# Kernel tuning notes

Hardware: AMD Instinct MI355X
Metric: run time of the kernel (lower is better)

Reference implementation:

```python
import jax, jax.numpy as jnp
import numpy as np

D_MODEL = 512
NUM_HEADS = 4
KEY_DIM = 512          # expand_k = 1.0
VALUE_DIM = 1024       # expand_v = 2.0
HEAD_QK = KEY_DIM // NUM_HEADS    # 128
HEAD_V = VALUE_DIM // NUM_HEADS   # 256
GATE_LOW_RANK = 16
GATE_LOGIT_NORMALIZER = 16
EPS = 1e-5
CHUNK = 64
B, HH, WW = 8, 56, 56
N = HH * WW


def rmsnorm(x, w, eps=EPS):
    return x * jax.lax.rsqrt(jnp.mean(x * x, axis=-1, keepdims=True) + eps) * w


def gla_chunk(q, k, v, gk, scale, chunk=CHUNK):
    """Chunked gated linear attention (causal, decay gate on key dim).
    q,k,gk: [B,H,N,dk], v: [B,H,N,dv]. Recurrence:
      S_t = diag(exp(gk_t)) S_{t-1} + k_t^T v_t ;  o_t = (q_t*scale) S_t
    """
    Bb, Hh, Nn, dk = q.shape
    dv = v.shape[-1]
    nc = Nn // chunk

    def rc(t):  # [B,H,N,d] -> [nc,B,H,chunk,d]
        return jnp.moveaxis(t.reshape(Bb, Hh, nc, chunk, t.shape[-1]), 2, 0)

    qs, ks, vs, gs = rc(q), rc(k), rc(v), rc(gk)
    b = jnp.cumsum(gs, axis=-2)  # inclusive intra-chunk log-decay
    mask = jnp.tril(jnp.ones((chunk, chunk), bool))

    def step(S, inp):
        q_, k_, v_, b_ = inp
        qe = q_ * jnp.exp(b_) * scale                      # [B,H,C,dk]
        A = jnp.einsum('bhtd,bhsd->bhts', qe, k_ * jnp.exp(-b_))
        A = jnp.where(mask, A, 0.0)                        # causal intra-chunk
        o = jnp.einsum('bhts,bhsv->bhtv', A, v_) \
            + jnp.einsum('bhtd,bhdv->bhtv', qe, S)         # inter-chunk
        btot = b_[..., -1:, :]                             # [B,H,1,dk]
        S = S * jnp.exp(btot[..., 0, :])[..., None] \
            + jnp.einsum('bhtd,bhtv->bhdv', k_ * jnp.exp(btot - b_), v_)
        return S, o

    S0 = jnp.zeros((Bb, Hh, dk, dv), q.dtype)
    _, os = jax.lax.scan(step, S0, (qs, ks, vs, b))
    return jnp.moveaxis(os, 0, 2).reshape(Bb, Hh, Nn, dv)


def setup_inputs() -> dict:
    key = jax.random.key(0)
    ks = jax.random.split(key, 9)
    s = 0.02
    return {
        'x': jax.random.normal(ks[0], (B, N, D_MODEL), jnp.float32),
        'conv_w': jax.random.normal(ks[1], (D_MODEL, 1, 3, 3), jnp.float32) * s,
        'qkv_w': jax.random.normal(ks[2], (2 * KEY_DIM + VALUE_DIM, D_MODEL), jnp.float32) * s,
        'gk_w1': jax.random.normal(ks[3], (GATE_LOW_RANK, D_MODEL), jnp.float32) * s,
        'gk_w2': jax.random.normal(ks[4], (2 * KEY_DIM, GATE_LOW_RANK), jnp.float32) * s,
        'gk_b2': jax.random.normal(ks[5], (2 * KEY_DIM,), jnp.float32) * s,
        'g_w': jax.random.normal(ks[6], (VALUE_DIM, D_MODEL), jnp.float32) * s,
        'g_b': jax.random.normal(ks[7], (VALUE_DIM,), jnp.float32) * s,
        'gnorm_w': jnp.ones((HEAD_V,), jnp.float32),
        'lnorm_w': jnp.ones((HEAD_V,), jnp.float32),
        'o_w': jax.random.normal(ks[8], (D_MODEL, VALUE_DIM), jnp.float32) * s,
        'hw_h': HH,
        'hw_w': WW,
    }


def reference(x, conv_w, qkv_w, gk_w1, gk_w2, gk_b2, g_w, g_b,
              gnorm_w, lnorm_w, o_w, hw_h, hw_w):
    Bb, Nn, C = x.shape
    # in_proj: depthwise 3x3 conv over spatial layout + SiLU
    x2d = x.reshape(Bb, hw_h, hw_w, C).transpose(0, 3, 1, 2)
    x2d = jax.lax.conv_general_dilated(
        x2d, conv_w, (1, 1), 'SAME',
        dimension_numbers=('NCHW', 'OIHW', 'NCHW'), feature_group_count=C)
    xs = jax.nn.silu(x2d).transpose(0, 2, 3, 1).reshape(Bb, Nn, C)

    qkv = xs @ qkv_w.T
    q, k, v = jnp.split(qkv, [KEY_DIM, 2 * KEY_DIM], axis=-1)

    def heads(t, d):  # [B,N,h*d] -> [B,h,N,d]
        return t.reshape(Bb, Nn, NUM_HEADS, d).transpose(0, 2, 1, 3)

    q, k, v = heads(q, HEAD_QK), heads(k, HEAD_QK), heads(v, HEAD_V)

    # low-rank gate projection, two groups (forward / backward scan)
    gk = (xs @ gk_w1.T) @ gk_w2.T + gk_b2
    gk = jax.nn.log_sigmoid(gk) / GATE_LOGIT_NORMALIZER
    gk_f, gk_b = jnp.split(gk, 2, axis=-1)
    gk_f, gk_b = heads(gk_f, HEAD_QK), heads(gk_b, HEAD_QK)

    scale = HEAD_QK ** -0.5
    o_f = gla_chunk(q, k, v, gk_f, scale)
    flip = lambda t: t[:, :, ::-1]
    o_b = flip(gla_chunk(flip(q), flip(k), flip(v), flip(gk_b), scale))

    o = rmsnorm(o_f, gnorm_w) + rmsnorm(o_b, lnorm_w)   # [B,h,N,dv]
    o = o.transpose(0, 2, 1, 3).reshape(Bb, Nn, VALUE_DIM)
    g = xs @ g_w.T + g_b
    o = jax.nn.silu(g) * o                              # swish output gate
    return o @ o_w.T
```

## Files before the change

kernel.cpp:

```cpp
#include <hip/hip_runtime.h>
#include <hip/hip_bf16.h>
#include <math.h>

#define NHEADS 4
#define DMODEL 512
#define HQK 128
#define HV 256
#define BBATCH 8
#define SH 56
#define SWW 56
#define SEQN (SH*SWW)
#define NTOK (BBATCH*SEQN)
#define CH2 32
#define NC2 (SEQN/CH2)


typedef __bf16 bf16x8 __attribute__((ext_vector_type(8)));
typedef float  f32x4  __attribute__((ext_vector_type(4)));

__device__ __forceinline__ float silu_f(float v){ return v / (1.f + __expf(-v)); }

__device__ __forceinline__ float b2f(unsigned short u){
  union { unsigned int i; float f; } c; c.i = ((unsigned int)u) << 16; return c.f;
}
__device__ __forceinline__ unsigned short f2b(float f){
  __bf16 h = (__bf16)f;
  unsigned short u; __builtin_memcpy(&u, &h, 2); return u;
}
__device__ __forceinline__ float h2f(unsigned short u){
  _Float16 h; __builtin_memcpy(&h, &u, 2); return (float)h;
}
__device__ __forceinline__ unsigned short f2h(float f){
  _Float16 h = (_Float16)f; unsigned short u; __builtin_memcpy(&u, &h, 2); return u;
}
__device__ __forceinline__ float lsig16(float z){
  float e = __expf(-fabsf(z));
  return (fminf(z, 0.f) - __logf(1.f + e)) * 0.0625f;
}
__device__ __forceinline__ void up8(uint4 v, unsigned short* o){
  o[0]=(unsigned short)v.x; o[1]=(unsigned short)(v.x>>16);
  o[2]=(unsigned short)v.y; o[3]=(unsigned short)(v.y>>16);
  o[4]=(unsigned short)v.z; o[5]=(unsigned short)(v.z>>16);
  o[6]=(unsigned short)v.w; o[7]=(unsigned short)(v.w>>16);
}
__device__ __forceinline__ uint4 pk8(const unsigned short* s){
  uint4 v;
  v.x = (unsigned)s[0] | ((unsigned)s[1]<<16);
  v.y = (unsigned)s[2] | ((unsigned)s[3]<<16);
  v.z = (unsigned)s[4] | ((unsigned)s[5]<<16);
  v.w = (unsigned)s[6] | ((unsigned)s[7]<<16);
  return v;
}

#define GLL16(gp, lp) __builtin_amdgcn_global_load_lds( \
    (const __attribute__((address_space(1))) unsigned int*)(gp), \
    (__attribute__((address_space(3))) unsigned int*)(lp), 16, 0, 0)

__global__ __launch_bounds__(256) void k_w2b(const float* __restrict__ w,
                                             unsigned short* __restrict__ o, int n){
  int i = (blockIdx.x*256 + threadIdx.x) << 2;
  if (i >= n) return;
  float4 v = *(const float4*)&w[i];
  ushort4 p;
  p.x = f2b(v.x); p.y = f2b(v.y); p.z = f2b(v.z); p.w = f2b(v.w);
  *(ushort4*)&o[i] = p;
}

__global__ __launch_bounds__(256) void k_wc(const float* __restrict__ w1,
                                            const float* __restrict__ w2,
                                            unsigned short* __restrict__ wc){
  int idx = blockIdx.x*256 + threadIdx.x;
  int n = idx >> 9, k = idx & 511;
  float acc = 0.f;
  #pragma unroll
  for (int r=0;r<16;++r) acc += w2[n*16+r]*w1[r*512+k];
  wc[idx] = f2b(acc);
}

__global__ __launch_bounds__(256) void k_conv_silu(const float* __restrict__ x,
                                                   const float* __restrict__ cw,
                                                   unsigned short* __restrict__ xs){
  int gid = blockIdx.x*256 + threadIdx.x;
  int c4  = (gid & 127) << 2;
  int tok = gid >> 7;
  int b = tok / SEQN, sp = tok % SEQN;
  int hh = sp / SWW, ww = sp % SWW;
  float a0=0.f,a1=0.f,a2=0.f,a3=0.f;
  #pragma unroll
  for (int dh=-1; dh<=1; ++dh){
    int h2 = hh+dh; if (h2<0||h2>=SH) continue;
    #pragma unroll
    for (int dw=-1; dw<=1; ++dw){
      int w2 = ww+dw; if (w2<0||w2>=SWW) continue;
      const float4 xv = *(const float4*)&x[((size_t)(b*SEQN + h2*SWW + w2))*DMODEL + c4];
      int tap = (dh+1)*3 + (dw+1);
      a0 += xv.x * cw[(c4+0)*9 + tap];
      a1 += xv.y * cw[(c4+1)*9 + tap];
      a2 += xv.z * cw[(c4+2)*9 + tap];
      a3 += xv.w * cw[(c4+3)*9 + tap];
    }
  }
  ushort4 o;
  o.x = f2b(silu_f(a0)); o.y = f2b(silu_f(a1)); o.z = f2b(silu_f(a2)); o.w = f2b(silu_f(a3));
  *(ushort4*)&xs[(size_t)tok*DMODEL + c4] = o;
}

template<int ACT, int CBF>
__global__ __launch_bounds__(256) void k_gemm_mfma(const unsigned short* __restrict__ A,
                                                   const unsigned short* __restrict__ W,
                                                   const float* __restrict__ bias,
                                                   void* __restrict__ Cv,
                                                   int M, int N, int K){
  __shared__ unsigned short sA[128*32];
  __shared__ unsigned short sB[128*32];
  const int tid  = threadIdx.x;
  const int wave = tid >> 6, lane = tid & 63;
  const int lm = lane & 15, quad = lane >> 4;
  const int wm = wave & 1, wn = wave >> 1;
  const int m0 = blockIdx.y * 128, n0 = blockIdx.x * 128;

  const int r0 = tid >> 2,  c0 = (tid & 3) << 3;
  const int f1 = tid + 256;
  const int r1 = f1 >> 2,   c1 = (f1 & 3) << 3;

  f32x4 acc[4][4] = {};

  for (int kt = 0; kt < K; kt += 32){
    GLL16(&A[(size_t)(m0 + r0)*K + kt + c0], &sA[(size_t)tid*8]);
    GLL16(&A[(size_t)(m0 + r1)*K + kt + c1], &sA[(size_t)f1*8]);
    GLL16(&W[(size_t)(n0 + r0)*K + kt + c0], &sB[(size_t)tid*8]);
    GLL16(&W[(size_t)(n0 + r1)*K + kt + c1], &sB[(size_t)f1*8]);
    __syncthreads();
    bf16x8 af[4], bf[4];
    #pragma unroll
    for (int i=0;i<4;++i) af[i] = *(const bf16x8*)&sA[(wm*64 + i*16 + lm)*32 + quad*8];
    #pragma unroll
    for (int j=0;j<4;++j) bf[j] = *(const bf16x8*)&sB[(wn*64 + j*16 + lm)*32 + quad*8];
    #pragma unroll
    for (int i=0;i<4;++i)
      #pragma unroll
      for (int j=0;j<4;++j)
        acc[i][j] = __builtin_amdgcn_mfma_f32_16x16x32_bf16(af[i], bf[j], acc[i][j], 0, 0, 0);
    __syncthreads();
  }

  #pragma unroll
  for (int i=0;i<4;++i){
    #pragma unroll
    for (int r=0;r<4;++r){
      size_t m = (size_t)(m0 + wm*64 + i*16 + quad*4 + r);
      #pragma unroll
      for (int j=0;j<4;++j){
        int n = n0 + wn*64 + j*16 + lm;
        float v = acc[i][j][r];
        if (bias) v += bias[n];
        if (ACT==1) v = silu_f(v);
        if (CBF) ((unsigned short*)Cv)[m*(size_t)N + n] = f2b(v);
        else     ((float*)Cv)[m*(size_t)N + n] = v;
      }
    }
  }
}

__global__ __launch_bounds__(256) void k_prep(unsigned short* __restrict__ qkv,
                                              const unsigned short* __restrict__ z,
                                              unsigned short* __restrict__ dbuf,
                                              unsigned short* __restrict__ ebF,
                                              unsigned short* __restrict__ ebB){
  const int blk = blockIdx.x;
  const int bb = blk / NC2, cB = blk % NC2;
  const int j  = threadIdx.x << 1;
  const int cb = j & 0x180;
  const int sl = j & 127;
  const int d1 = ((sl & 7) << 4) | (sl >> 3);
  const int d2 = d1 + 16;
  const size_t base = (size_t)bb*SEQN + cB*CH2;
  const float sc = 0.08838834764831845f;
  float bf0[CH2], bf1[CH2];
  float r0 = 0.f, r1 = 0.f;
  #pragma unroll
  for (int t=0;t<CH2;++t){
    size_t tok = base + t;
    float z0 = b2f(z[tok*1024 + cb + d1]);
    float z1 = b2f(z[tok*1024 + cb + d2]);
    r0 += lsig16(z0);
    r1 += lsig16(z1);
    bf0[t] = r0; bf1[t] = r1;
    float qv1 = b2f(qkv[tok*2048 + cb + d1]);
    float qv2 = b2f(qkv[tok*2048 + cb + d2]);
    float kv1 = b2f(qkv[tok*2048 + 512 + cb + d1]);
    float kv2 = b2f(qkv[tok*2048 + 512 + cb + d2]);
    float e0 = __expf(r0),  e1 = __expf(r1);
    float n0 = __expf(-r0), n1 = __expf(-r1);
    unsigned qo = (unsigned)f2b(qv1*e0*sc) | ((unsigned)f2b(qv2*e1*sc) << 16);
    unsigned ko = (unsigned)f2b(kv1*n0)    | ((unsigned)f2b(kv2*n1) << 16);
    __syncthreads();
    *(unsigned*)&qkv[tok*2048 + j] = qo;
    *(unsigned*)&qkv[tok*2048 + 512 + j] = ko;
  }
  const int hh = j >> 7;
  {
    int ef = ((bb*NHEADS + hh)*NC2 + cB)*HQK;
    ebF[ef + d1] = f2h(__expf(bf0[CH2-1]));
    ebF[ef + d2] = f2h(__expf(bf1[CH2-1]));
  }
  r0 = 0.f; r1 = 0.f;
  #pragma unroll
  for (int t=CH2-1;t>=0;--t){
    size_t tok = base + t;
    float z0 = b2f(z[tok*1024 + 512 + cb + d1]);
    float z1 = b2f(z[tok*1024 + 512 + cb + d2]);
    r0 += lsig16(z0);
    r1 += lsig16(z1);
    float dd0 = r0 - bf0[t], dd1 = r1 - bf1[t];
    *(unsigned*)&dbuf[tok*512 + j] = (unsigned)f2h(__expf(dd0))
                                   | ((unsigned)f2h(__expf(dd1)) << 16);
  }
  {
    int eb = ((bb*NHEADS + hh)*NC2 + (NC2-1-cB))*HQK;
    ebB[eb + d1] = f2h(__expf(r0));
    ebB[eb + d2] = f2h(__expf(r1));
  }
}

#define SKET_STORE(sKeT_, kb_, o8_, ts_) \
  _Pragma("unroll") \
  for (int u=0;u<8;++u){ \
    (sKeT_)[(u*16 + 2*(o8_)    )*40 + (ts_)] = (kb_)[u]; \
    (sKeT_)[(u*16 + 2*(o8_) + 1)*40 + (ts_)] = (kb_)[u+8]; \
  }

__global__ __launch_bounds__(256) void k_gla_state(const unsigned short* __restrict__ qkvb,
                                                   const unsigned short* __restrict__ dbuf,
                                                   const unsigned short* __restrict__ ebFt,
                                                   const unsigned short* __restrict__ ebBt,
                                                   float* __restrict__ dSseg){
  __shared__ __align__(16) unsigned short sKeT[128*40];
  __shared__ __align__(16) unsigned short sVT[64*40];
  __shared__ float sEb[128];

  const int tid = threadIdx.x;
  const int bx = blockIdx.x;
  const int combo = bx & 255, seg = bx >> 8;
  const int vq = combo & 3, dir = (combo>>2)&1, hh = (combo>>3)&3, bb = (combo>>5)&7;

  const int w = tid >> 6, lane = tid & 63;
  const int quad = lane >> 4, lm = lane & 15;
  const int ts = tid >> 3, o8 = tid & 7, d16 = o8 << 4;
  const int tl = tid & 31, vg = tid >> 5;

  const int kcol = 512 + hh*HQK, vcol = 1024 + hh*HV + vq*64;
  const int dcol = hh*HQK;
  const unsigned short* ebT = dir ? ebBt : ebFt;
  const int ebBase = (bb*NHEADS + hh)*NC2*HQK;
  const int c0 = (seg==0)?0:(seg==1)?13:(seg==2)?25:(seg==3)?37:(seg==4)?50:62;
  const int c1 = (seg==0)?13:(seg==1)?25:(seg==2)?37:(seg==3)?50:(seg==4)?62:74;

  f32x4 Sreg[8];
  #pragma unroll
  for (int i=0;i<8;++i){
    #pragma unroll
    for (int r=0;r<4;++r) Sreg[i][r] = 0.f;
  }

  for (int c = c0; c < c1; ++c){
    {
      int p = c*CH2 + ts;
      int n = dir ? (SEQN-1-p) : p;
      size_t tok = (size_t)bb*SEQN + n;
      uint4 k0 = *(const uint4*)&qkvb[tok*2048 + kcol + d16];
      uint4 k1 = *(const uint4*)&qkvb[tok*2048 + kcol + d16 + 8];
      unsigned short kb[16];
      up8(k0, kb); up8(k1, kb+8);
      if (dir){
        uint4 dd0 = *(const uint4*)&dbuf[tok*512 + dcol + d16];
        uint4 dd1 = *(const uint4*)&dbuf[tok*512 + dcol + d16 + 8];
        unsigned short eh[16];
        up8(dd0, eh); up8(dd1, eh+8);
        #pragma unroll
        for (int u=0;u<16;++u)
          kb[u] = f2b(b2f(kb[u]) * __builtin_amdgcn_rcpf(h2f(eh[u])));
      }
      SKET_STORE(sKeT, kb, o8, ts);
    }
    {
      int p = c*CH2 + tl;
      int n = dir ? (SEQN-1-p) : p;
      size_t tok = (size_t)bb*SEQN + n;
      uint4 uv = *(const uint4*)&qkvb[tok*2048 + vcol + vg*8];
      unsigned short su[8];
      up8(uv, su);
      #pragma unroll
      for (int u=0;u<8;++u) sVT[(vg*8+u)*40 + tl] = su[u];
    }
    if (tid < 128) sEb[tid] = h2f(ebT[ebBase + c*HQK + tid]);
    __syncthreads();
    bf16x8 vta = *(const bf16x8*)&sVT[(w*16+lm)*40 + quad*8];
    #pragma unroll
    for (int dt=0; dt<8; ++dt){
      bf16x8 kt = *(const bf16x8*)&sKeT[(dt*16+lm)*40 + quad*8];
      Sreg[dt] = __builtin_amdgcn_mfma_f32_16x16x32_bf16(vta, kt, Sreg[dt], 0, 0, 0);
      float eb = sEb[dt*16 + lm];
      #pragma unroll
      for (int r=0;r<4;++r) Sreg[dt][r] *= eb;
    }
    __syncthreads();
  }

  const size_t sbase = (size_t)bx * 8192;
  #pragma unroll
  for (int dt=0; dt<8; ++dt){
    #pragma unroll
    for (int r=0;r<4;++r)
      dSseg[sbase + (size_t)(w*16 + quad*4 + r)*128 + dt*16 + lm] = Sreg[dt][r];
  }
}

__global__ __launch_bounds__(256) void k_gla_comb(const float* __restrict__ dSseg,
                                                  float* __restrict__ dSf,
                                                  const unsigned short* __restrict__ ebFt,
                                                  const unsigned short* __restrict__ ebBt){
  const int combo = blockIdx.x;
  const int dir = (combo>>2)&1, hh = (combo>>3)&3, bb = (combo>>5)&7;
  const unsigned short* ebT = dir ? ebBt : ebFt;
  const int ebBase = (bb*NHEADS + hh)*NC2*HQK;
  const int t = threadIdx.x;
  const int d0 = (t << 2) & 127;
  float D1[4]={1,1,1,1}, D2[4]={1,1,1,1}, D3[4]={1,1,1,1}, D4[4]={1,1,1,1}, D5[4]={1,1,1,1};
  for (int c=13; c<25; ++c){
    ushort4 ev = *(const ushort4*)&ebT[ebBase + c*HQK + d0];
    D1[0]*=h2f(ev.x); D1[1]*=h2f(ev.y); D1[2]*=h2f(ev.z); D1[3]*=h2f(ev.w);
  }
  for (int c=25; c<37; ++c){
    ushort4 ev = *(const ushort4*)&ebT[ebBase + c*HQK + d0];
    D2[0]*=h2f(ev.x); D2[1]*=h2f(ev.y); D2[2]*=h2f(ev.z); D2[3]*=h2f(ev.w);
  }
  for (int c=37; c<50; ++c){
    ushort4 ev = *(const ushort4*)&ebT[ebBase + c*HQK + d0];
    D3[0]*=h2f(ev.x); D3[1]*=h2f(ev.y); D3[2]*=h2f(ev.z); D3[3]*=h2f(ev.w);
  }
  for (int c=50; c<62; ++c){
    ushort4 ev = *(const ushort4*)&ebT[ebBase + c*HQK + d0];
    D4[0]*=h2f(ev.x); D4[1]*=h2f(ev.y); D4[2]*=h2f(ev.z); D4[3]*=h2f(ev.w);
  }
  for (int c=62; c<74; ++c){
    ushort4 ev = *(const ushort4*)&ebT[ebBase + c*HQK + d0];
    D5[0]*=h2f(ev.x); D5[1]*=h2f(ev.y); D5[2]*=h2f(ev.z); D5[3]*=h2f(ev.w);
  }
  const size_t bA = (size_t)combo*8192;
  const size_t SEG = (size_t)256*8192;
  #pragma unroll
  for (int r=0;r<8;++r){
    int idx = r*1024 + (t<<2);
    float4 a0 = *(const float4*)&dSseg[bA + idx];
    float4 a1 = *(const float4*)&dSseg[bA + SEG + idx];
    float4 a2 = *(const float4*)&dSseg[bA + 2*SEG + idx];
    float4 a3 = *(const float4*)&dSseg[bA + 3*SEG + idx];
    float4 a4 = *(const float4*)&dSseg[bA + 4*SEG + idx];
    float4 a5 = *(const float4*)&dSseg[bA + 5*SEG + idx];
    float4 s25, s50, s74;
    s25.x = D1[0]*a0.x + a1.x; s25.y = D1[1]*a0.y + a1.y;
    s25.z = D1[2]*a0.z + a1.z; s25.w = D1[3]*a0.w + a1.w;
    s50.x = D3[0]*(D2[0]*s25.x + a2.x) + a3.x;
    s50.y = D3[1]*(D2[1]*s25.y + a2.y) + a3.y;
    s50.z = D3[2]*(D2[2]*s25.z + a2.z) + a3.z;
    s50.w = D3[3]*(D2[3]*s25.w + a2.w) + a3.w;
    s74.x = D5[0]*(D4[0]*s50.x + a4.x) + a5.x;
    s74.y = D5[1]*(D4[1]*s50.y + a4.y) + a5.y;
    s74.z = D5[2]*(D4[2]*s50.z + a4.z) + a5.z;
    s74.w = D5[3]*(D4[3]*s50.w + a4.w) + a5.w;
    *(float4*)&dSf[bA + idx] = s25;
    *(float4*)&dSf[SEG + bA + idx] = s50;
    *(float4*)&dSf[2*SEG + bA + idx] = s74;
  }
}

__global__ __launch_bounds__(256,2) void k_gla3(const unsigned short* __restrict__ qkvb,
                                                const unsigned short* __restrict__ dbuf,
                                                const unsigned short* __restrict__ ebFt,
                                                const unsigned short* __restrict__ ebBt,
                                                unsigned short* __restrict__ og,
                                                const float* __restrict__ dSf){
  __shared__ __align__(16) unsigned short sQe[32*136];
  __shared__ __align__(16) unsigned short sKe[32*136];
  __shared__ __align__(16) unsigned short sKeT[128*40];
  __shared__ __align__(16) unsigned short sVT[128*40];
  __shared__ __align__(16) unsigned short sST[128*136];
  __shared__ __align__(16) unsigned short sP[32*40];
  __shared__ float sEb[128];

  const int tid = threadIdx.x;
  const int bx = blockIdx.x;
  const int combo = bx & 127, seg = bx >> 7;
  const int vp = combo & 1, dir = (combo>>1)&1, hh = (combo>>2)&3, bb = (combo>>4)&7;

  const int w = tid >> 6, lane = tid & 63;
  const int quad = lane >> 4, lm = lane & 15;
  const int mt = w >> 1, nt = w & 1;
  const int ts = tid >> 3, o8 = tid & 7, d16 = o8 << 4;
  const int tl = tid & 31, vg = tid >> 5;

  const int qcol = hh*HQK, kcol = 512 + hh*HQK, vcol = 1024 + hh*HV + vp*128;
  const int dcol = hh*HQK;
  const unsigned short* ebT = dir ? ebBt : ebFt;
  const int ebBase = (bb*NHEADS + hh)*NC2*HQK;
  const size_t ogBase = ((size_t)((dir*BBATCH + bb)*NHEADS + hh)) * SEQN * HV;

  f32x4 Sreg[2][8];
  #pragma unroll
  for (int vh=0; vh<2; ++vh)
    #pragma unroll
    for (int i=0;i<8;++i)
      #pragma unroll
      for (int r=0;r<4;++r) Sreg[vh][i][r] = 0.f;
  if (seg){
    #pragma unroll
    for (int vh=0; vh<2; ++vh){
      const int combo_s = (vp*2+vh) | (dir<<2) | (hh<<3) | (bb<<5);
      const size_t sbase = ((size_t)(seg-1)*256 + combo_s) * 8192;
      #pragma unroll
      for (int dt=0; dt<8; ++dt){
        #pragma unroll
        for (int r=0;r<4;++r){
          float sv = dSf[sbase + (size_t)(w*16 + quad*4 + r)*128 + dt*16 + lm];
          Sreg[vh][dt][r] = sv;
          sST[(vh*64 + w*16 + quad*4 + r)*136 + lm*8 + dt] = f2b(sv);
        }
      }
    }
  } else {
    for (int i = tid; i < 128*136; i += 256) sST[i] = 0;
  }
  __syncthreads();

  const int cBeg = (seg==0)?0:(seg==1)?25:(seg==2)?50:74;
  const int cEnd = (seg==0)?25:(seg==1)?50:(seg==2)?74:98;

  for (int c = cBeg; c < cEnd; ++c){
    {
      int p = c*CH2 + ts;
      int n = dir ? (SEQN-1-p) : p;
      size_t tok = (size_t)bb*SEQN + n;
      uint4 q0 = *(const uint4*)&qkvb[tok*2048 + qcol + d16];
      uint4 q1 = *(const uint4*)&qkvb[tok*2048 + qcol + d16 + 8];
      uint4 k0 = *(const uint4*)&qkvb[tok*2048 + kcol + d16];
      uint4 k1 = *(const uint4*)&qkvb[tok*2048 + kcol + d16 + 8];
      unsigned short kb[16];
      up8(k0, kb); up8(k1, kb+8);
      if (dir){
        uint4 dd0 = *(const uint4*)&dbuf[tok*512 + dcol + d16];
        uint4 dd1 = *(const uint4*)&dbuf[tok*512 + dcol + d16 + 8];
        unsigned short eh[16], qb[16];
        up8(dd0, eh); up8(dd1, eh+8);
        up8(q0, qb);  up8(q1, qb+8);
        #pragma unroll
        for (int u=0;u<16;++u){
          float e  = h2f(eh[u]);
          float ei = __builtin_amdgcn_rcpf(e);
          qb[u] = f2b(b2f(qb[u]) * e);
          kb[u] = f2b(b2f(kb[u]) * ei);
        }
        q0 = pk8(qb); q1 = pk8(qb+8);
        k0 = pk8(kb); k1 = pk8(kb+8);
      }
      *(uint4*)&sQe[ts*136 + d16]     = q0;
      *(uint4*)&sQe[ts*136 + d16 + 8] = q1;
      *(uint4*)&sKe[ts*136 + d16]     = k0;
      *(uint4*)&sKe[ts*136 + d16 + 8] = k1;
      SKET_STORE(sKeT, kb, o8, ts);
      int pv = c*CH2 + tl;
      int nv = dir ? (SEQN-1-pv) : pv;
      size_t tokv = (size_t)bb*SEQN + nv;
      uint4 uv0 = *(const uint4*)&qkvb[tokv*2048 + vcol + vg*8];
      uint4 uv1 = *(const uint4*)&qkvb[tokv*2048 + vcol + 64 + vg*8];
      unsigned short su[8];
      up8(uv0, su);
      #pragma unroll
      for (int u=0;u<8;++u) sVT[(vg*8+u)*40 + tl] = su[u];
      up8(uv1, su);
      #pragma unroll
      for (int u=0;u<8;++u) sVT[(64+vg*8+u)*40 + tl] = su[u];
    }
    if (tid < 128) sEb[tid] = h2f(ebT[ebBase + c*HQK + tid]);
    __syncthreads();
    bf16x8 qf[2][4];
    #pragma unroll
    for (int tt=0; tt<2; ++tt){
      #pragma unroll
      for (int ks=0; ks<4; ++ks)
        qf[tt][ks] = *(const bf16x8*)&sQe[(tt*16+lm)*136 + ks*32 + quad*8];
    }
    f32x4 a1;
    #pragma unroll
    for (int r=0;r<4;++r) a1[r] = 0.f;
    #pragma unroll
    for (int ks=0; ks<4; ++ks){
      bf16x8 kfr = *(const bf16x8*)&sKe[(nt*16+lm)*136 + ks*32 + quad*8];
      a1 = __builtin_amdgcn_mfma_f32_16x16x32_bf16(qf[mt][ks], kfr, a1, 0, 0, 0);
    }
    f32x4 ot[2][2];
    #pragma unroll
    for (int vh=0; vh<2; ++vh)
      #pragma unroll
      for (int tt=0; tt<2; ++tt)
        #pragma unroll
        for (int r=0;r<4;++r) ot[vh][tt][r] = 0.f;
    #pragma unroll
    for (int ks=0; ks<4; ++ks){
      #pragma unroll
      for (int vh=0; vh<2; ++vh){
        bf16x8 stf = *(const bf16x8*)&sST[(vh*64 + w*16+lm)*136 + ks*32 + quad*8];
        #pragma unroll
        for (int tt=0; tt<2; ++tt)
          ot[vh][tt] = __builtin_amdgcn_mfma_f32_16x16x32_bf16(stf, qf[tt][ks], ot[vh][tt], 0, 0, 0);
      }
    }
    #pragma unroll
    for (int r=0;r<4;++r){
      int t = mt*16 + quad*4 + r, s = nt*16 + lm;
      sP[t*40 + s] = f2b((s <= t) ? a1[r] : 0.f);
    }
    __syncthreads();
    bf16x8 vta[2];
    vta[0] = *(const bf16x8*)&sVT[(w*16+lm)*40 + quad*8];
    vta[1] = *(const bf16x8*)&sVT[(64 + w*16+lm)*40 + quad*8];
    #pragma unroll
    for (int dt=0; dt<8; ++dt){
      bf16x8 kt = *(const bf16x8*)&sKeT[(dt*16+lm)*40 + quad*8];
      float eb = sEb[dt*16 + lm];
      #pragma unroll
      for (int vh=0; vh<2; ++vh){
        Sreg[vh][dt] = __builtin_amdgcn_mfma_f32_16x16x32_bf16(vta[vh], kt, Sreg[vh][dt], 0, 0, 0);
        #pragma unroll
        for (int r=0;r<4;++r) Sreg[vh][dt][r] *= eb;
      }
    }
    #pragma unroll
    for (int vh=0; vh<2; ++vh){
      #pragma unroll
      for (int r=0;r<4;++r){
        uint4 pkv;
        pkv.x = (unsigned)f2b(Sreg[vh][0][r]) | ((unsigned)f2b(Sreg[vh][1][r]) << 16);
        pkv.y = (unsigned)f2b(Sreg[vh][2][r]) | ((unsigned)f2b(Sreg[vh][3][r]) << 16);
        pkv.z = (unsigned)f2b(Sreg[vh][4][r]) | ((unsigned)f2b(Sreg[vh][5][r]) << 16);
        pkv.w = (unsigned)f2b(Sreg[vh][6][r]) | ((unsigned)f2b(Sreg[vh][7][r]) << 16);
        *(uint4*)&sST[(vh*64 + w*16 + quad*4 + r)*136 + lm*8] = pkv;
      }
    }
    #pragma unroll
    for (int tt=0; tt<2; ++tt){
      bf16x8 pf = *(const bf16x8*)&sP[(tt*16+lm)*40 + quad*8];
      int p = c*CH2 + tt*16 + lm;
      int n = dir ? (SEQN-1-p) : p;
      #pragma unroll
      for (int vh=0; vh<2; ++vh){
        ot[vh][tt] = __builtin_amdgcn_mfma_f32_16x16x32_bf16(vta[vh], pf, ot[vh][tt], 0, 0, 0);
        ushort4 o4;
        o4.x = f2b(ot[vh][tt][0]); o4.y = f2b(ot[vh][tt][1]);
        o4.z = f2b(ot[vh][tt][2]); o4.w = f2b(ot[vh][tt][3]);
        *(ushort4*)&og[ogBase + (size_t)n*HV + vp*128 + vh*64 + w*16 + quad*4] = o4;
      }
    }
    __syncthreads();
  }
}

__global__ __launch_bounds__(256) void k_gate(const unsigned short* __restrict__ og,
                                              const unsigned short* __restrict__ g,
                                              const float* __restrict__ gnw,
                                              const float* __restrict__ lnw,
                                              unsigned short* __restrict__ y){
  int tok = blockIdx.x;
  int bb = tok / SEQN, n = tok % SEQN;
  int hh = threadIdx.x >> 6, l = threadIdx.x & 63;
  int j4 = l << 2;
  size_t basef = ((size_t)((0*BBATCH+bb)*NHEADS+hh))*SEQN*HV + (size_t)n*HV + j4;
  size_t baseb = ((size_t)((1*BBATCH+bb)*NHEADS+hh))*SEQN*HV + (size_t)n*HV + j4;
  ushort4 ofu = *(const ushort4*)&og[basef];
  ushort4 obu = *(const ushort4*)&og[baseb];
  float of0=b2f(ofu.x), of1=b2f(ofu.y), of2=b2f(ofu.z), of3=b2f(ofu.w);
  float ob0=b2f(obu.x), ob1=b2f(obu.y), ob2=b2f(obu.z), ob3=b2f(obu.w);
  float ssf = of0*of0 + of1*of1 + of2*of2 + of3*of3;
  float ssb = ob0*ob0 + ob1*ob1 + ob2*ob2 + ob3*ob3;
  #pragma unroll
  for (int m=32;m>=1;m>>=1){ ssf += __shfl_xor(ssf,m,64); ssb += __shfl_xor(ssb,m,64); }
  float rf = rsqrtf(ssf*(1.f/HV) + 1e-5f);
  float rb = rsqrtf(ssb*(1.f/HV) + 1e-5f);
  float4 gn = *(const float4*)&gnw[j4];
  float4 ln = *(const float4*)&lnw[j4];
  ushort4 gvu = *(const ushort4*)&g[(size_t)tok*1024 + hh*HV + j4];
  float g0=b2f(gvu.x), g1=b2f(gvu.y), g2=b2f(gvu.z), g3=b2f(gvu.w);
  ushort4 out;
  out.x = f2b(g0*(of0*rf*gn.x + ob0*rb*ln.x));
  out.y = f2b(g1*(of1*rf*gn.y + ob1*rb*ln.y));
  out.z = f2b(g2*(of2*rf*gn.z + ob2*rb*ln.z));
  out.w = f2b(g3*(of3*rf*gn.w + ob3*rb*ln.w));
  *(ushort4*)&y[(size_t)tok*1024 + hh*HV + j4] = out;
}

extern "C" void kernel_launch(void* const* d_in, const int* in_sizes, int n_in,
                              void* d_out, int out_size, void* d_ws, size_t ws_size,
                              hipStream_t stream){
  (void)in_sizes; (void)n_in; (void)out_size;
  const float* x    = (const float*)d_in[0];
  const float* cw   = (const float*)d_in[1];
  const float* qkvw = (const float*)d_in[2];
  const float* gkw1 = (const float*)d_in[3];
  const float* gkw2 = (const float*)d_in[4];
  const float* gkb2 = (const float*)d_in[5];
  const float* gw   = (const float*)d_in[6];
  const float* gb   = (const float*)d_in[7];
  const float* gnw  = (const float*)d_in[8];
  const float* lnw  = (const float*)d_in[9];
  const float* ow   = (const float*)d_in[10];

  if (ws_size < 232816640u) return;
  char* wsb = (char*)d_ws;
  char* dob = (char*)d_out;
  unsigned short* qkv  = (unsigned short*)(wsb + 0);
  unsigned short* g    = (unsigned short*)(wsb + 51380224);
  unsigned short* og   = (unsigned short*)(wsb + 102760448);
  float*          dSseg= (float*)(wsb + 102760448);
  unsigned short* zbuf = (unsigned short*)(wsb + 102760448 + 25690112);
  unsigned short* wqb  = (unsigned short*)(wsb + 102760448 + 77070336);
  unsigned short* wc   = (unsigned short*)(wsb + 102760448 + 80216064);
  unsigned short* dbuf = (unsigned short*)(wsb + 205520896);
  unsigned short* wgb  = (unsigned short*)(wsb + 205520896);
  unsigned short* ebF  = (unsigned short*)(wsb + 231211008);
  unsigned short* ebB  = (unsigned short*)(wsb + 232013824);
  unsigned short* xs   = (unsigned short*)(dob + 0);
  float*          dSf  = (float*)(dob + 25690112);
  unsigned short* wob  = og;
  unsigned short* y    = qkv;
  float*          outp = (float*)d_out;

  k_conv_silu<<<NTOK*128/256, 256, 0, stream>>>(x, cw, xs);
  k_w2b<<<1024, 256, 0, stream>>>(qkvw, wqb, 2048*512);
  k_wc<<<2048, 256, 0, stream>>>(gkw1, gkw2, wc);
  k_gemm_mfma<0,1><<<dim3(16,196), 256, 0, stream>>>(xs, wqb, nullptr, qkv,  NTOK, 2048, 512);
  k_gemm_mfma<0,1><<<dim3(8,196),  256, 0, stream>>>(xs, wc,  gkb2,    zbuf, NTOK, 1024, 512);
  k_prep<<<BBATCH*NC2, 256, 0, stream>>>(qkv, zbuf, dbuf, ebF, ebB);
  k_gla_state<<<1536, 256, 0, stream>>>(qkv, dbuf, ebF, ebB, dSseg);
  k_gla_comb<<<256, 256, 0, stream>>>(dSseg, dSf, ebF, ebB);
  k_gla3<<<512, 256, 0, stream>>>(qkv, dbuf, ebF, ebB, og, dSf);
  k_w2b<<<512,  256, 0, stream>>>(gw, wgb, 1024*512);
  k_gemm_mfma<1,1><<<dim3(8,196),  256, 0, stream>>>(xs, wgb, gb, g, NTOK, 1024, 512);
  k_gate<<<NTOK, 256, 0, stream>>>(og, g, gnw, lnw, y);
  k_w2b<<<512, 256, 0, stream>>>(ow, wob, 512*1024);
  k_gemm_mfma<0,0><<<dim3(4,196), 256, 0, stream>>>(y, wob, nullptr, outp, NTOK, 512, 1024);
}
```

Before: 1.135 ms.

## Double-buffer GLA state kernel, widen V tile, and remap GEMM block order

The chunk-state kernel now has each block cover 128 value columns instead of 64, so the key tile and its decay scaling are loaded and computed once for twice the work, and the launch grid is halved. It double-buffers the shared-memory K/V/decay stages so the next chunk's loads are issued before the current chunk's MFMAs, leaving one barrier per iteration. Separately, the GEMM kernel remaps block indices across groups of eight, likely to spread neighbouring tiles across XCDs for better L2 locality. The risks are more shared memory and registers per block (launch bounds set to 3 blocks per CU) and fewer blocks to fill the GPU.

Measured after the change: 1.084 ms. -4.5%, faster.

```diff
diff --git a/kernel.cpp b/kernel.cpp
--- a/kernel.cpp
+++ b/kernel.cpp
@@ -117,7 +117,10 @@
   const int wave = tid >> 6, lane = tid & 63;
   const int lm = lane & 15, quad = lane >> 4;
   const int wm = wave & 1, wn = wave >> 1;
-  const int m0 = blockIdx.y * 128, n0 = blockIdx.x * 128;
+  const int nwg = gridDim.x * gridDim.y;
+  const int hb  = blockIdx.y * gridDim.x + blockIdx.x;
+  const int fb  = (hb & 7) * (nwg >> 3) + (hb >> 3);
+  const int m0 = (fb / gridDim.x) * 128, n0 = (fb % gridDim.x) * 128;
 
   const int r0 = tid >> 2,  c0 = (tid & 3) << 3;
   const int f1 = tid + 256;
@@ -230,89 +233,103 @@
     (sKeT_)[(u*16 + 2*(o8_) + 1)*40 + (ts_)] = (kb_)[u+8]; \
   }
 
-__global__ __launch_bounds__(256) void k_gla_state(const unsigned short* __restrict__ qkvb,
-                                                   const unsigned short* __restrict__ dbuf,
-                                                   const unsigned short* __restrict__ ebFt,
-                                                   const unsigned short* __restrict__ ebBt,
-                                                   float* __restrict__ dSseg){
-  __shared__ __align__(16) unsigned short sKeT[128*40];
-  __shared__ __align__(16) unsigned short sVT[64*40];
-  __shared__ float sEb[128];
+__global__ __launch_bounds__(256,3) void k_gla_state(const unsigned short* __restrict__ qkvb,
+                                                     const unsigned short* __restrict__ dbuf,
+                                                     const unsigned short* __restrict__ ebFt,
+                                                     const unsigned short* __restrict__ ebBt,
+                                                     float* __restrict__ dSseg){
+  __shared__ __align__(16) unsigned short sKeT[2][128*40];
+  __shared__ __align__(16) unsigned short sVT[2][128*40];
+  __shared__ float sEb[2][128];
 
   const int tid = threadIdx.x;
   const int bx = blockIdx.x;
-  const int combo = bx & 255, seg = bx >> 8;
-  const int vq = combo & 3, dir = (combo>>2)&1, hh = (combo>>3)&3, bb = (combo>>5)&7;
+  const int combo = bx & 127, seg = bx >> 7;
+  const int vp = combo & 1, dir = (combo>>1)&1, hh = (combo>>2)&3, bb = (combo>>4)&7;
 
   const int w = tid >> 6, lane = tid & 63;
   const int quad = lane >> 4, lm = lane & 15;
   const int ts = tid >> 3, o8 = tid & 7, d16 = o8 << 4;
   const int tl = tid & 31, vg = tid >> 5;
 
-  const int kcol = 512 + hh*HQK, vcol = 1024 + hh*HV + vq*64;
+  const int kcol = 512 + hh*HQK, vcol = 1024 + hh*HV + vp*128;
   const int dcol = hh*HQK;
   const unsigned short* ebT = dir ? ebBt : ebFt;
   const int ebBase = (bb*NHEADS + hh)*NC2*HQK;
   const int c0 = (seg==0)?0:(seg==1)?13:(seg==2)?25:(seg==3)?37:(seg==4)?50:62;
   const int c1 = (seg==0)?13:(seg==1)?25:(seg==2)?37:(seg==3)?50:(seg==4)?62:74;
 
-  f32x4 Sreg[8];
-  #pragma unroll
-  for (int i=0;i<8;++i){
-    #pragma unroll
-    for (int r=0;r<4;++r) Sreg[i][r] = 0.f;
-  }
-
+#define STSTAGE(c_, bi_) { \
+    int p_ = (c_)*CH2 + ts; \
+    int n_ = dir ? (SEQN-1-p_) : p_; \
+    size_t tok_ = (size_t)bb*SEQN + n_; \
+    uint4 k0_ = *(const uint4*)&qkvb[tok_*2048 + kcol + d16]; \
+    uint4 k1_ = *(const uint4*)&qkvb[tok_*2048 + kcol + d16 + 8]; \
+    unsigned short kb_[16]; \
+    up8(k0_, kb_); up8(k1_, kb_+8); \
+    if (dir){ \
+      uint4 dd0_ = *(const uint4*)&dbuf[tok_*512 + dcol + d16]; \
+      uint4 dd1_ = *(const uint4*)&dbuf[tok_*512 + dcol + d16 + 8]; \
+      unsigned short eh_[16]; \
+      up8(dd0_, eh_); up8(dd1_, eh_+8); \
+      _Pragma("unroll") \
+      for (int u=0;u<16;++u) \
+        kb_[u] = f2b(b2f(kb_[u]) * __builtin_amdgcn_rcpf(h2f(eh_[u]))); \
+    } \
+    SKET_STORE(sKeT[bi_], kb_, o8, ts); \
+    int pv_ = (c_)*CH2 + tl; \
+    int nv_ = dir ? (SEQN-1-pv_) : pv_; \
+    size_t tokv_ = (size_t)bb*SEQN + nv_; \
+    uint4 uv0_ = *(const uint4*)&qkvb[tokv_*2048 + vcol + vg*8]; \
+    uint4 uv1_ = *(const uint4*)&qkvb[tokv_*2048 + vcol + 64 + vg*8]; \
+    unsigned short su_[8]; \
+    up8(uv0_, su_); \
+    _Pragma("unroll") \
+    for (int u=0;u<8;++u) sVT[bi_][(vg*8+u)*40 + tl] = su_[u]; \
+    up8(uv1_, su_); \
+    _Pragma("unroll") \
+    for (int u=0;u<8;++u) sVT[bi_][(64+vg*8+u)*40 + tl] = su_[u]; \
+    if (tid < 128) sEb[bi_][tid] = h2f(ebT[ebBase + (c_)*HQK + tid]); \
+  }
+
+  f32x4 Sreg[2][8];
+  #pragma unroll
+  for (int vh=0; vh<2; ++vh)
+    #pragma unroll
+    for (int i=0;i<8;++i)
+      #pragma unroll
+      for (int r=0;r<4;++r) Sreg[vh][i][r] = 0.f;
+
+  STSTAGE(c0, 0);
+  __syncthreads();
   for (int c = c0; c < c1; ++c){
-    {
-      int p = c*CH2 + ts;
-      int n = dir ? (SEQN-1-p) : p;
-      size_t tok = (size_t)bb*SEQN + n;
-      uint4 k0 = *(const uint4*)&qkvb[tok*2048 + kcol + d16];
-      uint4 k1 = *(const uint4*)&qkvb[tok*2048 + kcol + d16 + 8];
-      unsigned short kb[16];
-      up8(k0, kb); up8(k1, kb+8);
-      if (dir){
-        uint4 dd0 = *(const uint4*)&dbuf[tok*512 + dcol + d16];
-        uint4 dd1 = *(const uint4*)&dbuf[tok*512 + dcol + d16 + 8];
-        unsigned short eh[16];
-        up8(dd0, eh); up8(dd1, eh+8);
-        #pragma unroll
-        for (int u=0;u<16;++u)
-          kb[u] = f2b(b2f(kb[u]) * __builtin_amdgcn_rcpf(h2f(eh[u])));
-      }
-      SKET_STORE(sKeT, kb, o8, ts);
-    }
-    {
-      int p = c*CH2 + tl;
-      int n = dir ? (SEQN-1-p) : p;
-      size_t tok = (size_t)bb*SEQN + n;
-      uint4 uv = *(const uint4*)&qkvb[tok*2048 + vcol + vg*8];
-      unsigned short su[8];
-      up8(uv, su);
-      #pragma unroll
-      for (int u=0;u<8;++u) sVT[(vg*8+u)*40 + tl] = su[u];
-    }
-    if (tid < 128) sEb[tid] = h2f(ebT[ebBase + c*HQK + tid]);
+    const int cur = (c - c0) & 1;
+    if (c + 1 < c1) STSTAGE(c+1, cur^1);
+    bf16x8 vta0 = *(const bf16x8*)&sVT[cur][(w*16+lm)*40 + quad*8];
+    bf16x8 vta1 = *(const bf16x8*)&sVT[cur][(64 + w*16+lm)*40 + quad*8];
+    #pragma unroll
+    for (int dt=0; dt<8; ++dt){
+      bf16x8 kt = *(const bf16x8*)&sKeT[cur][(dt*16+lm)*40 + quad*8];
+      float eb = sEb[cur][dt*16 + lm];
+      Sreg[0][dt] = __builtin_amdgcn_mfma_f32_16x16x32_bf16(vta0, kt, Sreg[0][dt], 0, 0, 0);
+      Sreg[1][dt] = __builtin_amdgcn_mfma_f32_16x16x32_bf16(vta1, kt, Sreg[1][dt], 0, 0, 0);
+      #pragma unroll
+      for (int r=0;r<4;++r){ Sreg[0][dt][r] *= eb; Sreg[1][dt][r] *= eb; }
+    }
     __syncthreads();
-    bf16x8 vta = *(const bf16x8*)&sVT[(w*16+lm)*40 + quad*8];
+  }
+#undef STSTAGE
+
+  #pragma unroll
+  for (int vh=0; vh<2; ++vh){
+    const int combo_s = (vp*2+vh) | (dir<<2) | (hh<<3) | (bb<<5);
+    const size_t sbase = ((size_t)seg*256 + combo_s) * 8192;
     #pragma unroll
     for (int dt=0; dt<8; ++dt){
-      bf16x8 kt = *(const bf16x8*)&sKeT[(dt*16+lm)*40 + quad*8];
-      Sreg[dt] = __builtin_amdgcn_mfma_f32_16x16x32_bf16(vta, kt, Sreg[dt], 0, 0, 0);
-      float eb = sEb[dt*16 + lm];
-      #pragma unroll
-      for (int r=0;r<4;++r) Sreg[dt][r] *= eb;
-    }
-    __syncthreads();
-  }
-
-  const size_t sbase = (size_t)bx * 8192;
-  #pragma unroll
-  for (int dt=0; dt<8; ++dt){
-    #pragma unroll
-    for (int r=0;r<4;++r)
-      dSseg[sbase + (size_t)(w*16 + quad*4 + r)*128 + dt*16 + lm] = Sreg[dt][r];
+      #pragma unroll
+      for (int r=0;r<4;++r)
+        dSseg[sbase + (size_t)(w*16 + quad*4 + r)*128 + dt*16 + lm] = Sreg[vh][dt][r];
+    }
   }
 }
 
@@ -640,7 +657,7 @@
   k_gemm_mfma<0,1><<<dim3(16,196), 256, 0, stream>>>(xs, wqb, nullptr, qkv,  NTOK, 2048, 512);
   k_gemm_mfma<0,1><<<dim3(8,196),  256, 0, stream>>>(xs, wc,  gkb2,    zbuf, NTOK, 1024, 512);
   k_prep<<<BBATCH*NC2, 256, 0, stream>>>(qkv, zbuf, dbuf, ebF, ebB);
-  k_gla_state<<<1536, 256, 0, stream>>>(qkv, dbuf, ebF, ebB, dSseg);
+  k_gla_state<<<768, 256, 0, stream>>>(qkv, dbuf, ebF, ebB, dSseg);
   k_gla_comb<<<256, 256, 0, stream>>>(dSseg, dSf, ebF, ebB);
   k_gla3<<<512, 256, 0, stream>>>(qkv, dbuf, ebF, ebB, og, dSf);
   k_w2b<<<512,  256, 0, stream>>>(gw, wgb, 1024*512);
```
